# Optimization experiments

Hardware: AMD Instinct MI355X
Metric: run time of the kernel (lower is better)

The kernel has to match this reference:

```python
import jax, jax.numpy as jnp
import numpy as np

B, T, D = 2, 2048, 1024
H = 16
HD = D // H


def setup_inputs() -> dict:
    key = jax.random.key(0)
    ks = jax.random.split(key, 9)
    s = 1.0 / np.sqrt(D)
    return {
        "x": jax.random.normal(ks[0], (B, T, D), dtype=jnp.float32),
        "Wq": jax.random.normal(ks[1], (D, D), dtype=jnp.float32) * s,
        "bq": jax.random.normal(ks[2], (D,), dtype=jnp.float32) * s,
        "Wk": jax.random.normal(ks[3], (D, D), dtype=jnp.float32) * s,
        "bk": jax.random.normal(ks[4], (D,), dtype=jnp.float32) * s,
        "Wv": jax.random.normal(ks[5], (D, D), dtype=jnp.float32) * s,
        "bv": jax.random.normal(ks[6], (D,), dtype=jnp.float32) * s,
        "Wo": jax.random.normal(ks[7], (D, D), dtype=jnp.float32) * s,
        "bo": jax.random.normal(ks[8], (D,), dtype=jnp.float32) * s,
    }


def reference(x, Wq, bq, Wk, bk, Wv, bv, Wo, bo):
    b, t, d = x.shape
    # projections; torch Linear computes x @ W.T + b
    def proj(W, bias):
        y = jnp.einsum("btd,ed->bte", x, W) + bias
        return y.reshape(b, t, H, HD).transpose(0, 2, 1, 3)  # [B,H,T,HD]
    q = proj(Wq, bq)
    k = proj(Wk, bk)
    v = proj(Wv, bv)
    scores = jnp.einsum("bhqd,bhkd->bhqk", q, k) / np.sqrt(HD)  # [B,H,T,T]
    causal = jnp.triu(jnp.ones((t, t), dtype=bool), k=1)
    scores = jnp.where(causal[None, None], jnp.float32(-1e9), scores)
    attn = jax.nn.softmax(scores, axis=-1)
    out = jnp.einsum("bhqk,bhkd->bhqd", attn, v)  # [B,H,T,HD]
    out = out.transpose(0, 2, 1, 3).reshape(b, t, d)
    return jnp.einsum("btd,ed->bte", out, Wo) + bo
```

## Files before the change

kernel.cpp:

```cpp
#include <hip/hip_runtime.h>


#define DEV __device__ __forceinline__

typedef __attribute__((ext_vector_type(8))) __bf16 bf16x8;
typedef __attribute__((ext_vector_type(4))) float f32x4;

DEV unsigned short f2bf(float f) {
  union { float f; unsigned u; } c;
  c.f = f;
  unsigned u = c.u + 0x7FFFu + ((c.u >> 16) & 1u);
  return (unsigned short)(u >> 16);
}

DEV unsigned cvtpk(float lo, float hi) {
  unsigned r;
  asm("v_cvt_pk_bf16_f32 %0, %1, %2" : "=v"(r) : "v"(lo), "v"(hi));
  return r;
}

DEV void gload16(const unsigned short* g, unsigned short* l) {
  __builtin_amdgcn_global_load_lds(
      (const __attribute__((address_space(1))) unsigned int*)g,
      (__attribute__((address_space(3))) unsigned int*)l, 16, 0, 0);
}

DEV f32x4 mfma16(bf16x8 a, bf16x8 b, f32x4 c) {
  return __builtin_amdgcn_mfma_f32_16x16x32_bf16(a, b, c, 0, 0, 0);
}

#define WAITVM(n) asm volatile("s_waitcnt vmcnt(" #n ")" ::: "memory")
#define WAITLGKM() asm volatile("s_waitcnt lgkmcnt(0)" ::: "memory")
#define BAR() __builtin_amdgcn_s_barrier()
#define SCHEDB() __builtin_amdgcn_sched_barrier(0)
#define PRIO(n) __builtin_amdgcn_s_setprio(n)

__global__ __launch_bounds__(256) void k_cvt_all(
    const float* __restrict__ x, const float* __restrict__ wq,
    const float* __restrict__ wk, const float* __restrict__ wv,
    const float* __restrict__ wo, unsigned short* __restrict__ dst) {
  int i = blockIdx.x * blockDim.x + threadIdx.x;
  const float* s;
  int off;
  if (i < 1048576) {
    s = x; off = i;
  } else {
    int j = i - 1048576;
    int w = j >> 18;
    off = j & 262143;
    s = (w == 0) ? wq : (w == 1) ? wk : (w == 2) ? wv : wo;
  }
  float4 v = reinterpret_cast<const float4*>(s)[off];
  uint2 o;
  o.x = (unsigned)f2bf(v.x) | ((unsigned)f2bf(v.y) << 16);
  o.y = (unsigned)f2bf(v.z) | ((unsigned)f2bf(v.w) << 16);
  reinterpret_cast<uint2*>(dst)[i] = o;
}

DEV void gemm_stage(const unsigned short* __restrict__ A,
                    const unsigned short* __restrict__ W,
                    unsigned short* la, unsigned short* lb,
                    int m0, int n0, int k0, int tid) {
#pragma unroll
  for (int i = 0; i < 2; ++i) {
    const int c = i * 256 + tid;
    const int row = c >> 2;
    const int scb = (((c & 3) << 4)) ^ ((row & 3) << 4);
    gload16(A + (m0 + row) * 1024 + k0 + (scb >> 1),
            (unsigned short*)((char*)la + c * 16));
    gload16(W + (n0 + row) * 1024 + k0 + (scb >> 1),
            (unsigned short*)((char*)lb + c * 16));
  }
}

DEV void gemm_core_128(const unsigned short* __restrict__ A,
                       const unsigned short* __restrict__ W,
                       unsigned short* la0, unsigned short* lb0,
                       int m0, int n0, f32x4 (&acc)[4][4]) {
  const int tid = threadIdx.x;
  const int lane = tid & 63;
  const int wave = tid >> 6;
  const int wm = (wave >> 1) * 64, wn = (wave & 1) * 64;
  const int g16 = ((lane >> 4) << 4);
  const int sx = (lane & 3) << 4;

  gemm_stage(A, W, la0, lb0, m0, n0, 0, tid);
  __syncthreads();

  for (int kt = 0; kt < 32; ++kt) {
    const int cur = kt & 1;
    unsigned short* la = la0 + cur * 4096;
    unsigned short* lb = lb0 + cur * 4096;
    if (kt + 1 < 32)
      gemm_stage(A, W, la0 + (cur ^ 1) * 4096, lb0 + (cur ^ 1) * 4096, m0, n0,
                 (kt + 1) * 32, tid);
    bf16x8 af[4], bfr[4];
#pragma unroll
    for (int m = 0; m < 4; ++m)
      af[m] = *reinterpret_cast<const bf16x8*>(
          (char*)la + (wm + m * 16 + (lane & 15)) * 64 + (g16 ^ sx));
#pragma unroll
    for (int n = 0; n < 4; ++n)
      bfr[n] = *reinterpret_cast<const bf16x8*>(
          (char*)lb + (wn + n * 16 + (lane & 15)) * 64 + (g16 ^ sx));
#pragma unroll
    for (int m = 0; m < 4; ++m)
#pragma unroll
      for (int n = 0; n < 4; ++n)
        acc[m][n] = mfma16(af[m], bfr[n], acc[m][n]);
    __syncthreads();
  }
}

__global__ __launch_bounds__(256) void k_gemm_qkv(
    const unsigned short* __restrict__ X, const unsigned short* __restrict__ Wq,
    const unsigned short* __restrict__ Wk, const unsigned short* __restrict__ Wv,
    const float* __restrict__ bq, const float* __restrict__ bk,
    const float* __restrict__ bv, unsigned short* __restrict__ Qo,
    unsigned short* __restrict__ Ko, unsigned short* __restrict__ Vo) {
  __shared__ unsigned short ls[16384];
  const int id = blockIdx.x;
  const int xcd = id & 7, s4 = id >> 3;
  const int mode = s4 >> 5;
  const int bx = ((s4 >> 3) & 3) * 2 + (xcd & 1);
  const int by = (s4 & 7) * 4 + (xcd >> 1);
  const unsigned short* W = (mode == 0) ? Wq : (mode == 1) ? Wk : Wv;
  const float* bias = (mode == 0) ? bq : (mode == 1) ? bk : bv;
  const int m0 = by * 128, n0 = bx * 128;
  f32x4 acc[4][4] = {};
  gemm_core_128(X, W, ls, ls + 8192, m0, n0, acc);

  const int lane = threadIdx.x & 63, wave = threadIdx.x >> 6;
  const int l15 = lane & 15, g = lane >> 4;
  const int wm = (wave >> 1) * 64, wn = (wave & 1) * 64;
  unsigned short* lw = ls + wave * 4096;

  const int h = (n0 + wn) >> 6;
  const int rbase0 = m0 + wm;
  const int b = rbase0 >> 11;
  const int tb0 = rbase0 & 2047;

  if (mode == 2) {
#pragma unroll
    for (int m = 0; m < 4; ++m)
#pragma unroll
      for (int n = 0; n < 4; ++n) {
        const float bb = bias[n0 + wn + n * 16 + l15];
        uint2 w;
        w.x = cvtpk(acc[m][n][0] + bb, acc[m][n][1] + bb);
        w.y = cvtpk(acc[m][n][2] + bb, acc[m][n][3] + bb);
        *reinterpret_cast<uint2*>(
            (char*)lw + (n * 16 + l15) * 128 +
            ((((m << 2) + g) ^ (l15 & 14)) << 3)) = w;
      }
    WAITLGKM();
    SCHEDB();
#pragma unroll
    for (int it = 0; it < 8; ++it) {
      const int hd = (lane >> 3) + it * 8;
      const int jj = ((lane & 7) << 1) ^ (hd & 14);
      uint4 v = *reinterpret_cast<const uint4*>((char*)lw + hd * 128 + jj * 8);
      *reinterpret_cast<uint4*>(
          &Vo[((((b << 4) + h) << 6) + hd) * 2048 + tb0 + ((lane & 7) << 3)]) =
          v;
    }
  } else {
    const float sc = (mode == 0) ? 0.180336880f : 1.0f;
#pragma unroll
    for (int m = 0; m < 4; ++m)
#pragma unroll
      for (int n = 0; n < 4; ++n) {
        const float bb = bias[n0 + wn + n * 16 + l15];
#pragma unroll
        for (int r = 0; r < 4; ++r)
          lw[(m * 16 + (g << 2) + r) * 64 + n * 16 + l15] =
              f2bf((acc[m][n][r] + bb) * sc);
      }
    WAITLGKM();
    SCHEDB();
    unsigned short* dst = (mode == 0) ? Qo : Ko;
#pragma unroll
    for (int it = 0; it < 8; ++it) {
      const int rr = (lane >> 3) + it * 8;
      const int ck = (lane & 7) * 8;
      uint4 v = *reinterpret_cast<const uint4*>(&lw[rr * 64 + ck]);
      *reinterpret_cast<uint4*>(
          &dst[(((b << 4) + h) * 2048 + tb0 + rr) * 64 + ck]) = v;
    }
  }
}

__global__ __launch_bounds__(256) void k_gemm_out(
    const unsigned short* __restrict__ Ctx, const unsigned short* __restrict__ Wo,
    const float* __restrict__ bo, float* __restrict__ Out) {
  __shared__ unsigned short ls[16384];
  unsigned short* la0 = ls;
  unsigned short* lb0 = ls + 8192;
  const int id = blockIdx.x;
  const int xcd = id & 7, s4 = id >> 3;
  const int bx = ((s4 >> 3) & 7) * 2 + (xcd & 1);
  const int by = (s4 & 7) * 4 + (xcd >> 1);
  const int tid = threadIdx.x;
  const int lane = tid & 63, wave = tid >> 6;
  const int l15 = lane & 15, g = lane >> 4;
  const int m0 = by * 128, n0 = bx * 64;
  const int wm = (wave >> 1) * 64, wn = (wave & 1) * 32;
  const int g16 = (g << 4);
  const int sx = (lane & 3) << 4;
  f32x4 acc[4][2] = {};

#define STG_OUT(buf, k0)                                                     \
  {                                                                          \
    _Pragma("unroll") for (int i = 0; i < 2; ++i) {                          \
      const int c = i * 256 + tid;                                           \
      const int row = c >> 2;                                                \
      const int scb = (((c & 3) << 4)) ^ ((row & 3) << 4);                   \
      gload16(Ctx + (m0 + row) * 1024 + (k0) + (scb >> 1),                   \
              (unsigned short*)((char*)(la0 + (buf)*4096) + c * 16));        \
    }                                                                        \
    {                                                                        \
      const int row = tid >> 2;                                              \
      const int scb = (((tid & 3) << 4)) ^ ((row & 3) << 4);                 \
      gload16(Wo + (n0 + row) * 1024 + (k0) + (scb >> 1),                    \
              (unsigned short*)((char*)(lb0 + (buf)*2048) + tid * 16));      \
    }                                                                        \
  }

  STG_OUT(0, 0);
  __syncthreads();

  for (int kt = 0; kt < 32; ++kt) {
    const int cur = kt & 1;
    unsigned short* la = la0 + cur * 4096;
    unsigned short* lb = lb0 + cur * 2048;
    if (kt + 1 < 32) STG_OUT(cur ^ 1, (kt + 1) * 32);
    bf16x8 af[4], bfr[2];
#pragma unroll
    for (int m = 0; m < 4; ++m)
      af[m] = *reinterpret_cast<const bf16x8*>(
          (char*)la + (wm + m * 16 + l15) * 64 + (g16 ^ sx));
#pragma unroll
    for (int n = 0; n < 2; ++n)
      bfr[n] = *reinterpret_cast<const bf16x8*>(
          (char*)lb + (wn + n * 16 + l15) * 64 + (g16 ^ sx));
#pragma unroll
    for (int m = 0; m < 4; ++m)
#pragma unroll
      for (int n = 0; n < 2; ++n)
        acc[m][n] = mfma16(af[m], bfr[n], acc[m][n]);
    __syncthreads();
  }
#undef STG_OUT

  float* lwf = (float*)(ls + wave * 4096);
#pragma unroll
  for (int m = 0; m < 4; ++m)
#pragma unroll
    for (int n = 0; n < 2; ++n) {
      const float bb = bo[n0 + wn + n * 16 + l15];
#pragma unroll
      for (int r = 0; r < 4; ++r)
        lwf[(m * 16 + (g << 2) + r) * 32 + n * 16 + l15] = acc[m][n][r] + bb;
    }
  WAITLGKM();
  SCHEDB();
#pragma unroll
  for (int it = 0; it < 8; ++it) {
    const int rr = (lane >> 3) + it * 8;
    const int ck = (lane & 7) * 4;
    float4 v = *reinterpret_cast<const float4*>(&lwf[rr * 32 + ck]);
    *reinterpret_cast<float4*>(&Out[(m0 + wm + rr) * 1024 + n0 + wn + ck]) = v;
  }
}


DEV void attn_stage(const unsigned short* __restrict__ Kb,
                    const unsigned short* __restrict__ Vb,
                    unsigned short* lk, unsigned short* lv, int kv0, int tid) {
  const int c = tid;
  const int row = c >> 3;
  const int cb = (c & 7) << 4;
  const int scb = cb ^ ((row & 7) << 4);
  gload16(Kb + (kv0 + row) * 64 + (scb >> 1),
          (unsigned short*)((char*)lk + c * 16));
  gload16(Vb + row * 2048 + kv0 + (scb >> 1),
          (unsigned short*)((char*)lv + c * 16));
}

DEV void attn_step(const unsigned short* lk, const unsigned short* lv,
                   unsigned short (&lp)[16][72], const bf16x8 (&qf)[2],
                   f32x4 (&o)[4], float& lsum, int lane, int qloc, bool diag) {
  const int g = lane >> 4;
  f32x4 st[4];
  PRIO(1);
#pragma unroll
  for (int n = 0; n < 4; ++n) {
    f32x4 z = {};
    const int row = n * 16 + (lane & 15);
    const int sw = (row & 7) << 4;
#pragma unroll
    for (int kk = 0; kk < 2; ++kk) {
      bf16x8 kf = *reinterpret_cast<const bf16x8*>(
          (char*)lk + row * 128 + ((kk * 64 + (g << 4)) ^ sw));
      z = mfma16(kf, qf[kk], z);
    }
    st[n] = z;
  }
  PRIO(0);
  if (diag) {
#pragma unroll
    for (int n = 0; n < 4; ++n)
#pragma unroll
      for (int r = 0; r < 4; ++r)
        if (n * 16 + g * 4 + r > qloc) st[n][r] = -1e30f;
  }
  float rs = 0.f;
#pragma unroll
  for (int n = 0; n < 4; ++n)
#pragma unroll
    for (int r = 0; r < 4; ++r) {
      float p = exp2f(st[n][r]);
      st[n][r] = p;
      rs += p;
    }
  lsum += rs;
#pragma unroll
  for (int n = 0; n < 4; ++n) {
    uint2 w;
    w.x = cvtpk(st[n][0], st[n][1]);
    w.y = cvtpk(st[n][2], st[n][3]);
    *reinterpret_cast<uint2*>(&lp[lane & 15][n * 16 + g * 4]) = w;
  }
  WAITLGKM();
  SCHEDB();
  bf16x8 pb[2];
  pb[0] = *reinterpret_cast<const bf16x8*>(&lp[lane & 15][g * 8]);
  pb[1] = *reinterpret_cast<const bf16x8*>(&lp[lane & 15][32 + g * 8]);
  PRIO(1);
#pragma unroll
  for (int h = 0; h < 4; ++h) {
    const int row = h * 16 + (lane & 15);
    const int sw = (row & 7) << 4;
#pragma unroll
    for (int kk = 0; kk < 2; ++kk) {
      bf16x8 vf = *reinterpret_cast<const bf16x8*>(
          (char*)lv + row * 128 + ((kk * 64 + (g << 4)) ^ sw));
      o[h] = mfma16(vf, pb[kk], o[h]);
    }
  }
  PRIO(0);
}

DEV void attn_epi(unsigned short* __restrict__ Ctx,
                  unsigned short (&lp)[16][72], const f32x4 (&o)[4],
                  float lsum, int b, int hh, int qbase, int lane) {
  float lt = lsum;
  lt += __shfl_xor(lt, 16);
  lt += __shfl_xor(lt, 32);
  const float inv = 1.f / lt;
  const int g = lane >> 4;
#pragma unroll
  for (int h = 0; h < 4; ++h) {
    uint2 w;
    w.x = cvtpk(o[h][0] * inv, o[h][1] * inv);
    w.y = cvtpk(o[h][2] * inv, o[h][3] * inv);
    *reinterpret_cast<uint2*>(&lp[lane & 15][h * 16 + g * 4]) = w;
  }
  WAITLGKM();
  SCHEDB();
#pragma unroll
  for (int it = 0; it < 2; ++it) {
    const int q = (lane >> 3) + it * 8;
    const int ck = (lane & 7) * 8;
    uint4 v = *reinterpret_cast<const uint4*>(&lp[q][ck]);
    *reinterpret_cast<uint4*>(
        &Ctx[(b * 2048 + qbase + q) * 1024 + hh * 64 + ck]) = v;
  }
}

__global__ __launch_bounds__(512) void k_attn(
    const unsigned short* __restrict__ Q, const unsigned short* __restrict__ K,
    const unsigned short* __restrict__ Vt, unsigned short* __restrict__ Ctx) {
  __shared__ unsigned short lk[3 * 4096];
  __shared__ unsigned short lv[3 * 4096];
  __shared__ unsigned short lp[8][16][72];

  const int tid = threadIdx.x, lane = tid & 63, wave = tid >> 6;
  const int id = blockIdx.x;
  const int xcd = id & 7, r4 = id >> 3;
  const int ip = r4 & 15;
  const int bh = ((r4 >> 4) << 3) + xcd;

  const int qtA = ip;
  const int qtB = 31 - ip;
  const int nt = qtB + 1;

  const bool isB = wave < 4;
  const int wv4 = wave & 3;
  const int qt = isB ? qtB : qtA;
  const int myNt = isB ? nt : qtA + 1;

  const unsigned short* Kb = K + bh * 2048 * 64;
  const unsigned short* Vb = Vt + bh * 64 * 2048;

  bf16x8 qf[2];
  {
    const unsigned short* qr =
        Q + (bh * 2048 + qt * 64 + wv4 * 16 + (lane & 15)) * 64 +
        ((lane >> 4) << 3);
    qf[0] = *reinterpret_cast<const bf16x8*>(qr);
    qf[1] = *reinterpret_cast<const bf16x8*>(qr + 32);
  }

  f32x4 o[4] = {};
  float lsum = 0.f;
  const int qloc = wv4 * 16 + (lane & 15);

  attn_stage(Kb, Vb, lk, lv, 0, tid);
  attn_stage(Kb, Vb, lk + 4096, lv + 4096, 64, tid);
  WAITVM(2);
  BAR();

  for (int t = 0; t < nt; ++t) {
    const int nx = (t + 2 < nt) ? t + 2 : nt - 1;
    attn_stage(Kb, Vb, lk + ((t + 2) % 3) * 4096, lv + ((t + 2) % 3) * 4096,
               nx * 64, tid);
    WAITVM(4);
    BAR();
    SCHEDB();
    if (t < myNt)
      attn_step(lk + (t % 3) * 4096, lv + (t % 3) * 4096, lp[wave], qf, o,
                lsum, lane, qloc, t == qt);
    BAR();
  }

  WAITVM(0);

  const int b = bh >> 4, hh = bh & 15;
  attn_epi(Ctx, lp[wave], o, lsum, b, hh, qt * 64 + wv4 * 16, lane);
}

extern "C" void kernel_launch(void* const* d_in, const int* in_sizes, int n_in,
                              void* d_out, int out_size, void* d_ws,
                              size_t ws_size, hipStream_t stream) {
  const float* x = (const float*)d_in[0];
  const float* Wq = (const float*)d_in[1];
  const float* bq = (const float*)d_in[2];
  const float* Wk = (const float*)d_in[3];
  const float* bk = (const float*)d_in[4];
  const float* Wv = (const float*)d_in[5];
  const float* bv = (const float*)d_in[6];
  const float* Wo = (const float*)d_in[7];
  const float* bo = (const float*)d_in[8];
  float* out = (float*)d_out;

  char* ws = (char*)d_ws;
  unsigned short* xb = (unsigned short*)(ws);
  unsigned short* wqb = (unsigned short*)(ws + (8u << 20));
  unsigned short* wkb = (unsigned short*)(ws + (10u << 20));
  unsigned short* wvb = (unsigned short*)(ws + (12u << 20));
  unsigned short* wob = (unsigned short*)(ws + (14u << 20));
  unsigned short* Qb = (unsigned short*)(ws + (16u << 20));
  unsigned short* Kb = (unsigned short*)(ws + (24u << 20));
  unsigned short* Vtb = (unsigned short*)(ws + (32u << 20));
  unsigned short* Ctx = (unsigned short*)(ws + (40u << 20));

  k_cvt_all<<<8192, 256, 0, stream>>>(x, Wq, Wk, Wv, Wo, xb);

  k_gemm_qkv<<<768, 256, 0, stream>>>(xb, wqb, wkb, wvb, bq, bk, bv,
                                      Qb, Kb, Vtb);
  k_attn<<<512, 512, 0, stream>>>(Qb, Kb, Vtb, Ctx);
  k_gemm_out<<<512, 256, 0, stream>>>(Ctx, wob, bo, out);
}
```

Baseline: 115.9 us.

## Widen output GEMM tile to 128x128 via shared core, trim attention barriers

The output projection now uses a shared 128x128 GEMM core with 256 blocks instead of its own 128x64 tile loop. The epilogue writes fp32 results straight to global memory instead of staging them through LDS for coalesced stores. The attention loop moves its wait and barrier ahead of the prefetch and drops the trailing barrier, so one barrier per K/V tile replaces two. The larger tile reuses more data per block, but halves the block count, and the direct stores are less coalesced.

```diff
diff --git a/kernel.cpp b/kernel.cpp
--- a/kernel.cpp
+++ b/kernel.cpp
@@ -194,82 +194,28 @@
     const unsigned short* __restrict__ Ctx, const unsigned short* __restrict__ Wo,
     const float* __restrict__ bo, float* __restrict__ Out) {
   __shared__ unsigned short ls[16384];
-  unsigned short* la0 = ls;
-  unsigned short* lb0 = ls + 8192;
   const int id = blockIdx.x;
   const int xcd = id & 7, s4 = id >> 3;
-  const int bx = ((s4 >> 3) & 7) * 2 + (xcd & 1);
+  const int bx = ((s4 >> 3) & 3) * 2 + (xcd & 1);
   const int by = (s4 & 7) * 4 + (xcd >> 1);
-  const int tid = threadIdx.x;
-  const int lane = tid & 63, wave = tid >> 6;
+  const int m0 = by * 128, n0 = bx * 128;
+  f32x4 acc[4][4] = {};
+  gemm_core_128(Ctx, Wo, ls, ls + 8192, m0, n0, acc);
+
+  const int lane = threadIdx.x & 63, wave = threadIdx.x >> 6;
   const int l15 = lane & 15, g = lane >> 4;
-  const int m0 = by * 128, n0 = bx * 64;
-  const int wm = (wave >> 1) * 64, wn = (wave & 1) * 32;
-  const int g16 = (g << 4);
-  const int sx = (lane & 3) << 4;
-  f32x4 acc[4][2] = {};
-
-#define STG_OUT(buf, k0)                                                     \
-  {                                                                          \
-    _Pragma("unroll") for (int i = 0; i < 2; ++i) {                          \
-      const int c = i * 256 + tid;                                           \
-      const int row = c >> 2;                                                \
-      const int scb = (((c & 3) << 4)) ^ ((row & 3) << 4);                   \
-      gload16(Ctx + (m0 + row) * 1024 + (k0) + (scb >> 1),                   \
-              (unsigned short*)((char*)(la0 + (buf)*4096) + c * 16));        \
-    }                                                                        \
-    {                                                                        \
-      const int row = tid >> 2;                                              \
-      const int scb = (((tid & 3) << 4)) ^ ((row & 3) << 4);                 \
-      gload16(Wo + (n0 + row) * 1024 + (k0) + (scb >> 1),                    \
-              (unsigned short*)((char*)(lb0 + (buf)*2048) + tid * 16));      \
-    }                                                                        \
-  }
-
-  STG_OUT(0, 0);
-  __syncthreads();
-
-  for (int kt = 0; kt < 32; ++kt) {
-    const int cur = kt & 1;
-    unsigned short* la = la0 + cur * 4096;
-    unsigned short* lb = lb0 + cur * 2048;
-    if (kt + 1 < 32) STG_OUT(cur ^ 1, (kt + 1) * 32);
-    bf16x8 af[4], bfr[2];
-#pragma unroll
-    for (int m = 0; m < 4; ++m)
-      af[m] = *reinterpret_cast<const bf16x8*>(
-          (char*)la + (wm + m * 16 + l15) * 64 + (g16 ^ sx));
-#pragma unroll
-    for (int n = 0; n < 2; ++n)
-      bfr[n] = *reinterpret_cast<const bf16x8*>(
-          (char*)lb + (wn + n * 16 + l15) * 64 + (g16 ^ sx));
-#pragma unroll
-    for (int m = 0; m < 4; ++m)
-#pragma unroll
-      for (int n = 0; n < 2; ++n)
-        acc[m][n] = mfma16(af[m], bfr[n], acc[m][n]);
-    __syncthreads();
-  }
-#undef STG_OUT
-
-  float* lwf = (float*)(ls + wave * 4096);
-#pragma unroll
-  for (int m = 0; m < 4; ++m)
-#pragma unroll
-    for (int n = 0; n < 2; ++n) {
-      const float bb = bo[n0 + wn + n * 16 + l15];
+  const int wm = (wave >> 1) * 64, wn = (wave & 1) * 64;
+#pragma unroll
+  for (int m = 0; m < 4; ++m) {
+    const int rbase = m0 + wm + m * 16 + (g << 2);
+#pragma unroll
+    for (int n = 0; n < 4; ++n) {
+      const int col = n0 + wn + n * 16 + l15;
+      const float bb = bo[col];
 #pragma unroll
       for (int r = 0; r < 4; ++r)
-        lwf[(m * 16 + (g << 2) + r) * 32 + n * 16 + l15] = acc[m][n][r] + bb;
-    }
-  WAITLGKM();
-  SCHEDB();
-#pragma unroll
-  for (int it = 0; it < 8; ++it) {
-    const int rr = (lane >> 3) + it * 8;
-    const int ck = (lane & 7) * 4;
-    float4 v = *reinterpret_cast<const float4*>(&lwf[rr * 32 + ck]);
-    *reinterpret_cast<float4*>(&Out[(m0 + wm + rr) * 1024 + n0 + wn + ck]) = v;
+        Out[(rbase + r) * 1024 + col] = acc[m][n][r] + bb;
+    }
   }
 }
 
@@ -418,20 +364,19 @@
 
   attn_stage(Kb, Vb, lk, lv, 0, tid);
   attn_stage(Kb, Vb, lk + 4096, lv + 4096, 64, tid);
-  WAITVM(2);
-  BAR();
 
   for (int t = 0; t < nt; ++t) {
-    const int nx = (t + 2 < nt) ? t + 2 : nt - 1;
-    attn_stage(Kb, Vb, lk + ((t + 2) % 3) * 4096, lv + ((t + 2) % 3) * 4096,
-               nx * 64, tid);
-    WAITVM(4);
+    WAITVM(2);
     BAR();
+    {
+      const int nx = (t + 2 < nt) ? t + 2 : nt - 1;
+      attn_stage(Kb, Vb, lk + ((t + 2) % 3) * 4096, lv + ((t + 2) % 3) * 4096,
+                 nx * 64, tid);
+    }
     SCHEDB();
     if (t < myNt)
       attn_step(lk + (t % 3) * 4096, lv + (t % 3) * 4096, lp[wave], qf, o,
                 lsum, lane, qloc, t == qt);
-    BAR();
   }
 
   WAITVM(0);
@@ -470,5 +415,5 @@
   k_gemm_qkv<<<768, 256, 0, stream>>>(xb, wqb, wkb, wvb, bq, bk, bv,
                                       Qb, Kb, Vtb);
   k_attn<<<512, 512, 0, stream>>>(Qb, Kb, Vtb, Ctx);
-  k_gemm_out<<<512, 256, 0, stream>>>(Ctx, wob, bo, out);
-}
+  k_gemm_out<<<256, 256, 0, stream>>>(Ctx, wob, bo, out);
+}
```

After: 118.0 us. About the same (+1.8%).

## Stage 128-key KV blocks with double buffering and one barrier per block

Applied to the files above, without the earlier changes.

The attention loop now loads 128-key K/V tiles into two LDS buffers instead of 64-key tiles in a triple buffer. Each tile is processed as two 64-key sub-steps, which halves the number of barrier and wait points per key. The per-wave P scratch drops its padding in favour of an XOR swizzle to avoid bank conflicts. The trade-off is shallower prefetch: it waits for all outstanding loads (vmcnt 0) before each block, so load latency may be less well hidden.

```diff
diff --git a/kernel.cpp b/kernel.cpp
--- a/kernel.cpp
+++ b/kernel.cpp
@@ -274,34 +274,41 @@
 }
 
 
-DEV void attn_stage(const unsigned short* __restrict__ Kb,
-                    const unsigned short* __restrict__ Vb,
-                    unsigned short* lk, unsigned short* lv, int kv0, int tid) {
-  const int c = tid;
-  const int row = c >> 3;
-  const int cb = (c & 7) << 4;
-  const int scb = cb ^ ((row & 7) << 4);
-  gload16(Kb + (kv0 + row) * 64 + (scb >> 1),
-          (unsigned short*)((char*)lk + c * 16));
-  gload16(Vb + row * 2048 + kv0 + (scb >> 1),
-          (unsigned short*)((char*)lv + c * 16));
-}
-
-DEV void attn_step(const unsigned short* lk, const unsigned short* lv,
-                   unsigned short (&lp)[16][72], const bf16x8 (&qf)[2],
+DEV void attn_stage128(const unsigned short* __restrict__ Kb,
+                       const unsigned short* __restrict__ Vb,
+                       unsigned short* lk, unsigned short* lv, int kv0,
+                       int tid) {
+#pragma unroll
+  for (int i = 0; i < 2; ++i) {
+    const int c = i * 512 + tid;
+    const int krow = c >> 3;
+    const int kscb = ((c & 7) << 4) ^ ((krow & 7) << 4);
+    gload16(Kb + (kv0 + krow) * 64 + (kscb >> 1),
+            (unsigned short*)((char*)lk + c * 16));
+    const int vrow = c >> 4;
+    const int vscb = ((c & 15) << 4) ^ ((vrow & 7) << 4);
+    gload16(Vb + vrow * 2048 + kv0 + (vscb >> 1),
+            (unsigned short*)((char*)lv + c * 16));
+  }
+}
+
+DEV void attn_step(const unsigned short* lk128, int s,
+                   const unsigned short* lv128,
+                   unsigned short (&lp)[16][64], const bf16x8 (&qf)[2],
                    f32x4 (&o)[4], float& lsum, int lane, int qloc, bool diag) {
   const int g = lane >> 4;
+  const int l15 = lane & 15;
   f32x4 st[4];
   PRIO(1);
 #pragma unroll
   for (int n = 0; n < 4; ++n) {
     f32x4 z = {};
-    const int row = n * 16 + (lane & 15);
+    const int row = n * 16 + l15;
     const int sw = (row & 7) << 4;
 #pragma unroll
     for (int kk = 0; kk < 2; ++kk) {
       bf16x8 kf = *reinterpret_cast<const bf16x8*>(
-          (char*)lk + row * 128 + ((kk * 64 + (g << 4)) ^ sw));
+          (char*)lk128 + (s * 64 + row) * 128 + ((kk * 64 + (g << 4)) ^ sw));
       z = mfma16(kf, qf[kk], z);
     }
     st[n] = z;
@@ -324,27 +331,31 @@
       rs += p;
     }
   lsum += rs;
+  const int psw = (l15 & 7) << 4;
 #pragma unroll
   for (int n = 0; n < 4; ++n) {
     uint2 w;
     w.x = cvtpk(st[n][0], st[n][1]);
     w.y = cvtpk(st[n][2], st[n][3]);
-    *reinterpret_cast<uint2*>(&lp[lane & 15][n * 16 + g * 4]) = w;
+    *reinterpret_cast<uint2*>(
+        (char*)lp + l15 * 128 + (((n << 5) | (g << 3)) ^ psw)) = w;
   }
   WAITLGKM();
   SCHEDB();
   bf16x8 pb[2];
-  pb[0] = *reinterpret_cast<const bf16x8*>(&lp[lane & 15][g * 8]);
-  pb[1] = *reinterpret_cast<const bf16x8*>(&lp[lane & 15][32 + g * 8]);
+  pb[0] = *reinterpret_cast<const bf16x8*>(
+      (char*)lp + l15 * 128 + (((g << 4)) ^ psw));
+  pb[1] = *reinterpret_cast<const bf16x8*>(
+      (char*)lp + l15 * 128 + ((64 + (g << 4)) ^ psw));
   PRIO(1);
 #pragma unroll
   for (int h = 0; h < 4; ++h) {
-    const int row = h * 16 + (lane & 15);
-    const int sw = (row & 7) << 4;
+    const int vr = h * 16 + l15;
+    const int sw = (vr & 7) << 4;
 #pragma unroll
     for (int kk = 0; kk < 2; ++kk) {
       bf16x8 vf = *reinterpret_cast<const bf16x8*>(
-          (char*)lv + row * 128 + ((kk * 64 + (g << 4)) ^ sw));
+          (char*)lv128 + vr * 256 + ((s * 128 + kk * 64 + (g << 4)) ^ sw));
       o[h] = mfma16(vf, pb[kk], o[h]);
     }
   }
@@ -352,38 +363,41 @@
 }
 
 DEV void attn_epi(unsigned short* __restrict__ Ctx,
-                  unsigned short (&lp)[16][72], const f32x4 (&o)[4],
+                  unsigned short (&lp)[16][64], const f32x4 (&o)[4],
                   float lsum, int b, int hh, int qbase, int lane) {
   float lt = lsum;
   lt += __shfl_xor(lt, 16);
   lt += __shfl_xor(lt, 32);
   const float inv = 1.f / lt;
   const int g = lane >> 4;
+  const int l15 = lane & 15;
+  const int psw = (l15 & 7) << 4;
 #pragma unroll
   for (int h = 0; h < 4; ++h) {
     uint2 w;
     w.x = cvtpk(o[h][0] * inv, o[h][1] * inv);
     w.y = cvtpk(o[h][2] * inv, o[h][3] * inv);
-    *reinterpret_cast<uint2*>(&lp[lane & 15][h * 16 + g * 4]) = w;
+    *reinterpret_cast<uint2*>(
+        (char*)lp + l15 * 128 + (((h << 5) | (g << 3)) ^ psw)) = w;
   }
   WAITLGKM();
   SCHEDB();
 #pragma unroll
   for (int it = 0; it < 2; ++it) {
     const int q = (lane >> 3) + it * 8;
-    const int ck = (lane & 7) * 8;
-    uint4 v = *reinterpret_cast<const uint4*>(&lp[q][ck]);
+    const int blk = (lane & 7) ^ (q & 7);
+    uint4 v = *reinterpret_cast<const uint4*>((char*)lp + q * 128 + blk * 16);
     *reinterpret_cast<uint4*>(
-        &Ctx[(b * 2048 + qbase + q) * 1024 + hh * 64 + ck]) = v;
+        &Ctx[(b * 2048 + qbase + q) * 1024 + hh * 64 + ((lane & 7) << 3)]) = v;
   }
 }
 
 __global__ __launch_bounds__(512) void k_attn(
     const unsigned short* __restrict__ Q, const unsigned short* __restrict__ K,
     const unsigned short* __restrict__ Vt, unsigned short* __restrict__ Ctx) {
-  __shared__ unsigned short lk[3 * 4096];
-  __shared__ unsigned short lv[3 * 4096];
-  __shared__ unsigned short lp[8][16][72];
+  __shared__ unsigned short lk[2][8192];
+  __shared__ unsigned short lv[2][8192];
+  __shared__ unsigned short lp[8][16][64];
 
   const int tid = threadIdx.x, lane = tid & 63, wave = tid >> 6;
   const int id = blockIdx.x;
@@ -393,12 +407,11 @@
 
   const int qtA = ip;
   const int qtB = 31 - ip;
-  const int nt = qtB + 1;
+  const int nb = (qtB >> 1) + 1;
 
   const bool isB = wave < 4;
   const int wv4 = wave & 3;
   const int qt = isB ? qtB : qtA;
-  const int myNt = isB ? nt : qtA + 1;
 
   const unsigned short* Kb = K + bh * 2048 * 64;
   const unsigned short* Vb = Vt + bh * 64 * 2048;
@@ -416,22 +429,24 @@
   float lsum = 0.f;
   const int qloc = wv4 * 16 + (lane & 15);
 
-  attn_stage(Kb, Vb, lk, lv, 0, tid);
-  attn_stage(Kb, Vb, lk + 4096, lv + 4096, 64, tid);
-  WAITVM(2);
-  BAR();
-
-  for (int t = 0; t < nt; ++t) {
-    const int nx = (t + 2 < nt) ? t + 2 : nt - 1;
-    attn_stage(Kb, Vb, lk + ((t + 2) % 3) * 4096, lv + ((t + 2) % 3) * 4096,
-               nx * 64, tid);
-    WAITVM(4);
+  attn_stage128(Kb, Vb, lk[0], lv[0], 0, tid);
+
+  for (int t = 0; t < nb; ++t) {
+    WAITVM(0);
     BAR();
+    {
+      const int nx = (t + 1 < nb) ? t + 1 : nb - 1;
+      attn_stage128(Kb, Vb, lk[(t + 1) & 1], lv[(t + 1) & 1], nx * 128, tid);
+    }
     SCHEDB();
-    if (t < myNt)
-      attn_step(lk + (t % 3) * 4096, lv + (t % 3) * 4096, lp[wave], qf, o,
-                lsum, lane, qloc, t == qt);
-    BAR();
+    const unsigned short* lkc = lk[t & 1];
+    const unsigned short* lvc = lv[t & 1];
+#pragma unroll
+    for (int s = 0; s < 2; ++s) {
+      const int sub = 2 * t + s;
+      if (sub <= qt)
+        attn_step(lkc, s, lvc, lp[wave], qf, o, lsum, lane, qloc, sub == qt);
+    }
   }
 
   WAITVM(0);
```

Measured after the change: 110.7 us. 4.5% less time.
